# Performance work log

Hardware: AMD Instinct MI355X
Metric: run time of the kernel (lower is better)

The kernel has to match this reference:

```python
import jax, jax.numpy as jnp
import numpy as np

N_NODES = 50000
N_EDGES = 800000
IN_NODE = 128
IN_EDGE = 64
HEADS = 8
OUT_DIM = 8
HID = HEADS * OUT_DIM


def setup_inputs() -> dict:
    key = jax.random.key(0)
    ks = jax.random.split(key, 12)
    s = 1.0 / np.sqrt(IN_NODE)
    se = 1.0 / np.sqrt(IN_EDGE)
    return {
        "edge_index": jax.random.randint(ks[0], (2, N_EDGES), 0, N_NODES, dtype=jnp.int64),
        "h": jax.random.normal(ks[1], (N_NODES, IN_NODE), dtype=jnp.float32),
        "e": jax.random.normal(ks[2], (N_EDGES, IN_EDGE), dtype=jnp.float32),
        "WQ": jax.random.normal(ks[3], (IN_NODE, HID), dtype=jnp.float32) * s,
        "bQ": jnp.zeros((HID,), dtype=jnp.float32),
        "WK": jax.random.normal(ks[4], (IN_NODE, HID), dtype=jnp.float32) * s,
        "bK": jnp.zeros((HID,), dtype=jnp.float32),
        "WV": jax.random.normal(ks[5], (IN_NODE, HID), dtype=jnp.float32) * s,
        "bV": jnp.zeros((HID,), dtype=jnp.float32),
        "We": jax.random.normal(ks[6], (IN_EDGE, HID), dtype=jnp.float32) * se,
        "be": jnp.zeros((HID,), dtype=jnp.float32),
    }


def reference(edge_index, h, e, WQ, bQ, WK, bK, WV, bV, We, be):
    n = h.shape[0]
    # node projections -> [N, H, D]
    Q = (h @ WQ + bQ).reshape(-1, HEADS, OUT_DIM)
    K = (h @ WK + bK).reshape(-1, HEADS, OUT_DIM)
    V = (h @ WV + bV).reshape(-1, HEADS, OUT_DIM)
    pe = (e @ We + be).reshape(-1, HEADS, OUT_DIM)  # [E, H, D]

    src = edge_index[0]
    dst = edge_index[1]

    # per-edge attention score: K[src] * Q[dst] / sqrt(D) + proj_e
    score = (K[src] * Q[dst]) / np.sqrt(OUT_DIM) + pe  # [E, H, D]
    e_out = score
    a = jnp.exp(jnp.clip(score.sum(-1, keepdims=True), -5.0, 5.0))  # [E, H, 1]

    # scatter-sum of weighted V and scatter-mean of attention weights (by src)
    wV = jax.ops.segment_sum(V[src] * a, src, num_segments=n)       # [N, H, D]
    z_sum = jax.ops.segment_sum(a, src, num_segments=n)             # [N, H, 1]
    cnt = jax.ops.segment_sum(jnp.ones((src.shape[0],), a.dtype), src, num_segments=n)
    z = z_sum / jnp.maximum(cnt, 1.0)[:, None, None]                # scatter-mean

    h_out = wV / (z + 1e-06)
    return (h_out, e_out)
```

## Files before the change

### kernel.cpp

```cpp
#include <hip/hip_runtime.h>
#include <hip/hip_bf16.h>

typedef float  f32x4  __attribute__((ext_vector_type(4)));
typedef short  bf16x8 __attribute__((ext_vector_type(8)));

#define HEADS 8
#define HID 64
#define IN_NODE 128
#define IN_EDGE 64
#define LDSP 68

static __device__ __forceinline__ short f2bf(float f) {
    unsigned u = __builtin_bit_cast(unsigned, f);
    unsigned r = (u + 0x7FFFu + ((u >> 16) & 1u)) >> 16;
    return (short)r;
}

__global__ __launch_bounds__(256, 4) void qkv_kernel(
    const float* __restrict__ h,
    const float* __restrict__ WQ, const float* __restrict__ bQ,
    const float* __restrict__ WK, const float* __restrict__ bK,
    const float* __restrict__ WV, const float* __restrict__ bV,
    float* __restrict__ Q, float* __restrict__ K, float* __restrict__ V,
    int n_nodes)
{
    const int lane = threadIdx.x & 63;
    const int r16  = lane & 15;
    const int g4   = lane >> 4;
    const int wave   = blockIdx.x * (blockDim.x >> 6) + (threadIdx.x >> 6);
    const int nwaves = gridDim.x * (blockDim.x >> 6);
    const int mat  = blockIdx.y;

    const float* __restrict__ W  = (mat == 0) ? WQ : (mat == 1) ? WK : WV;
    const float* __restrict__ bp = (mat == 0) ? bQ : (mat == 1) ? bK : bV;
    float* __restrict__ out      = (mat == 0) ? Q  : (mat == 1) ? K  : V;

    bf16x8 bfr[4][4];
#pragma unroll
    for (int ct = 0; ct < 4; ++ct)
#pragma unroll
        for (int kc = 0; kc < 4; ++kc)
#pragma unroll
            for (int j = 0; j < 8; ++j) {
                int k = kc * 32 + g4 * 8 + j;
                bfr[ct][kc][j] = f2bf(W[k * HID + ct * 16 + r16]);
            }
    float bias[4];
#pragma unroll
    for (int ct = 0; ct < 4; ++ct) bias[ct] = bp[ct * 16 + r16];

    const int ntiles = (n_nodes + 15) >> 4;
    for (int tile = wave; tile < ntiles; tile += nwaves) {
        const int row0 = tile * 16;
        int arow = row0 + r16; if (arow > n_nodes - 1) arow = n_nodes - 1;
        const float* ap = h + (size_t)arow * IN_NODE + g4 * 8;

        bf16x8 afr[4];
#pragma unroll
        for (int kc = 0; kc < 4; ++kc) {
            f32x4 p0 = *reinterpret_cast<const f32x4*>(ap + kc * 32);
            f32x4 p1 = *reinterpret_cast<const f32x4*>(ap + kc * 32 + 4);
            afr[kc][0] = f2bf(p0.x); afr[kc][1] = f2bf(p0.y);
            afr[kc][2] = f2bf(p0.z); afr[kc][3] = f2bf(p0.w);
            afr[kc][4] = f2bf(p1.x); afr[kc][5] = f2bf(p1.y);
            afr[kc][6] = f2bf(p1.z); afr[kc][7] = f2bf(p1.w);
        }

        f32x4 acc[4] = {};
#pragma unroll
        for (int ct = 0; ct < 4; ++ct)
#pragma unroll
            for (int kc = 0; kc < 4; ++kc)
                acc[ct] = __builtin_amdgcn_mfma_f32_16x16x32_bf16(
                    afr[kc], bfr[ct][kc], acc[ct], 0, 0, 0);

#pragma unroll
        for (int ct = 0; ct < 4; ++ct)
#pragma unroll
            for (int r = 0; r < 4; ++r) {
                int orow = row0 + g4 * 4 + r;
                if (orow < n_nodes)
                    out[(size_t)orow * HID + ct * 16 + r16] = acc[ct][r] + bias[ct];
            }
    }
}

__global__ __launch_bounds__(256, 4) void edge_kernel(
    const int* __restrict__ ei, const float* __restrict__ e,
    const float* __restrict__ We, const float* __restrict__ be,
    const float* __restrict__ Q, const float* __restrict__ K,
    float* __restrict__ e_out, float* __restrict__ z_sum,
    float* __restrict__ cnt, int n_edges)
{
    const int lane = threadIdx.x & 63;
    const int wid  = threadIdx.x >> 6;
    const int r16  = lane & 15;
    const int g4   = lane >> 4;
    const int el   = lane >> 2;
    const int qg   = lane & 3;

    __shared__ float plds[4][16][LDSP];
    float (*my)[LDSP] = plds[wid];

    const int wave   = blockIdx.x * 4 + wid;
    const int nwaves = gridDim.x * 4;

    bf16x8 bfr[4][2];
#pragma unroll
    for (int ct = 0; ct < 4; ++ct)
#pragma unroll
        for (int kc = 0; kc < 2; ++kc)
#pragma unroll
            for (int j = 0; j < 8; ++j) {
                int k = kc * 32 + g4 * 8 + j;
                bfr[ct][kc][j] = f2bf(We[k * HID + ct * 16 + r16]);
            }
    float bias[4];
#pragma unroll
    for (int ct = 0; ct < 4; ++ct) bias[ct] = be[ct * 16 + r16];

    const float SC = 0.35355339059327373f;
    const int ntiles = (n_edges + 15) >> 4;
    for (int tile = wave; tile < ntiles; tile += nwaves) {
        const int e0 = tile * 16;

        int arow = e0 + r16; if (arow > n_edges - 1) arow = n_edges - 1;
        const float* ap = e + (size_t)arow * IN_EDGE + g4 * 8;
        f32x4 p0a = __builtin_nontemporal_load(reinterpret_cast<const f32x4*>(ap));
        f32x4 p1a = __builtin_nontemporal_load(reinterpret_cast<const f32x4*>(ap + 4));
        f32x4 p0b = __builtin_nontemporal_load(reinterpret_cast<const f32x4*>(ap + 32));
        f32x4 p1b = __builtin_nontemporal_load(reinterpret_cast<const f32x4*>(ap + 36));

        bf16x8 afr[2];
        afr[0][0] = f2bf(p0a.x); afr[0][1] = f2bf(p0a.y);
        afr[0][2] = f2bf(p0a.z); afr[0][3] = f2bf(p0a.w);
        afr[0][4] = f2bf(p1a.x); afr[0][5] = f2bf(p1a.y);
        afr[0][6] = f2bf(p1a.z); afr[0][7] = f2bf(p1a.w);
        afr[1][0] = f2bf(p0b.x); afr[1][1] = f2bf(p0b.y);
        afr[1][2] = f2bf(p0b.z); afr[1][3] = f2bf(p0b.w);
        afr[1][4] = f2bf(p1b.x); afr[1][5] = f2bf(p1b.y);
        afr[1][6] = f2bf(p1b.z); afr[1][7] = f2bf(p1b.w);

        f32x4 acc[4] = {};
#pragma unroll
        for (int ct = 0; ct < 4; ++ct) {
            acc[ct] = __builtin_amdgcn_mfma_f32_16x16x32_bf16(afr[0], bfr[ct][0], acc[ct], 0, 0, 0);
            acc[ct] = __builtin_amdgcn_mfma_f32_16x16x32_bf16(afr[1], bfr[ct][1], acc[ct], 0, 0, 0);
        }

#pragma unroll
        for (int ct = 0; ct < 4; ++ct)
#pragma unroll
            for (int r = 0; r < 4; ++r)
                my[g4 * 4 + r][ct * 16 + r16] = acc[ct][r] + bias[ct];

        int erow = e0 + el;
        bool valid = erow < n_edges;
        int erc = valid ? erow : n_edges - 1;
        int src = ei[erc];
        int dst = ei[n_edges + erc];

        const float* Kp = K + (size_t)src * HID + qg * 16;
        const float* Qp = Q + (size_t)dst * HID + qg * 16;
        f32x4 k0 = *reinterpret_cast<const f32x4*>(Kp);
        f32x4 k1 = *reinterpret_cast<const f32x4*>(Kp + 4);
        f32x4 k2 = *reinterpret_cast<const f32x4*>(Kp + 8);
        f32x4 k3 = *reinterpret_cast<const f32x4*>(Kp + 12);
        f32x4 q0 = *reinterpret_cast<const f32x4*>(Qp);
        f32x4 q1 = *reinterpret_cast<const f32x4*>(Qp + 4);
        f32x4 q2 = *reinterpret_cast<const f32x4*>(Qp + 8);
        f32x4 q3 = *reinterpret_cast<const f32x4*>(Qp + 12);

        asm volatile("s_waitcnt lgkmcnt(0)" ::: "memory");
        const float* mrow = &my[el][qg * 16];
        f32x4 p0 = *reinterpret_cast<const f32x4*>(mrow);
        f32x4 p1 = *reinterpret_cast<const f32x4*>(mrow + 4);
        f32x4 p2 = *reinterpret_cast<const f32x4*>(mrow + 8);
        f32x4 p3 = *reinterpret_cast<const f32x4*>(mrow + 12);

        f32x4 s0 = k0 * q0 * SC + p0;
        f32x4 s1 = k1 * q1 * SC + p1;
        f32x4 s2 = k2 * q2 * SC + p2;
        f32x4 s3 = k3 * q3 * SC + p3;

        if (valid) {
            float* op = e_out + (size_t)erow * HID + qg * 16;
            __builtin_nontemporal_store(s0, reinterpret_cast<f32x4*>(op));
            __builtin_nontemporal_store(s1, reinterpret_cast<f32x4*>(op + 4));
            __builtin_nontemporal_store(s2, reinterpret_cast<f32x4*>(op + 8));
            __builtin_nontemporal_store(s3, reinterpret_cast<f32x4*>(op + 12));
        }

        float hs0 = ((s0.x + s0.y) + (s0.z + s0.w)) + ((s1.x + s1.y) + (s1.z + s1.w));
        float hs1 = ((s2.x + s2.y) + (s2.z + s2.w)) + ((s3.x + s3.y) + (s3.z + s3.w));
        float a0 = __expf(fminf(fmaxf(hs0, -5.0f), 5.0f));
        float a1 = __expf(fminf(fmaxf(hs1, -5.0f), 5.0f));
        if (valid) {
            atomicAdd(&z_sum[src * HEADS + qg * 2], a0);
            atomicAdd(&z_sum[src * HEADS + qg * 2 + 1], a1);
            if (qg == 0) atomicAdd(&cnt[src], 1.0f);
        }
    }
}

__global__ __launch_bounds__(256) void finalize_kernel(
    const float* __restrict__ V, const float* __restrict__ z_sum,
    const float* __restrict__ cnt, float* __restrict__ h_out, int total)
{
    int i = blockIdx.x * 256 + threadIdx.x;
    if (i >= total) return;
    int node = i >> 6;
    int head = (i >> 3) & 7;
    float S = z_sum[node * HEADS + head];
    float c = fmaxf(cnt[node], 1.0f);
    h_out[i] = V[i] * S / (S / c + 1e-6f);
}

extern "C" void kernel_launch(void* const* d_in, const int* in_sizes, int n_in,
                              void* d_out, int out_size, void* d_ws, size_t ws_size,
                              hipStream_t stream)
{
    const int*   ei = (const int*)d_in[0];
    const float* h  = (const float*)d_in[1];
    const float* e  = (const float*)d_in[2];
    const float* WQ = (const float*)d_in[3];
    const float* bQ = (const float*)d_in[4];
    const float* WK = (const float*)d_in[5];
    const float* bK = (const float*)d_in[6];
    const float* WV = (const float*)d_in[7];
    const float* bV = (const float*)d_in[8];
    const float* We = (const float*)d_in[9];
    const float* be = (const float*)d_in[10];

    const int n_nodes = in_sizes[1] / IN_NODE;
    const int n_edges = in_sizes[2] / IN_EDGE;

    float* out_h = (float*)d_out;
    float* out_e = out_h + (size_t)n_nodes * HID;

    float* Q     = (float*)d_ws;
    float* K     = Q + (size_t)n_nodes * HID;
    float* V     = K + (size_t)n_nodes * HID;
    float* z_sum = V + (size_t)n_nodes * HID;
    float* cnt   = z_sum + (size_t)n_nodes * HEADS;

    (void)hipMemsetAsync(z_sum, 0, (size_t)n_nodes * (HEADS + 1) * sizeof(float), stream);

    {
        dim3 grid(96, 3);
        qkv_kernel<<<grid, 256, 0, stream>>>(h, WQ, bQ, WK, bK, WV, bV,
                                             Q, K, V, n_nodes);
    }
    {
        edge_kernel<<<2048, 256, 0, stream>>>(ei, e, We, be, Q, K,
                                              out_e, z_sum, cnt, n_edges);
    }
    {
        const int total = n_nodes * HID;
        finalize_kernel<<<(total + 255) / 256, 256, 0, stream>>>(V, z_sum, cnt,
                                                                 out_h, total);
    }
}
```

Before: 243.7 us.

## Split scatter atomics out of edge kernel into separate z-pass kernel

```diff
diff --git a/kernel.cpp b/kernel.cpp
--- a/kernel.cpp
+++ b/kernel.cpp
@@ -1,6 +1,7 @@
 #include <hip/hip_runtime.h>
 #include <hip/hip_bf16.h>
 
+typedef float  f32x2  __attribute__((ext_vector_type(2)));
 typedef float  f32x4  __attribute__((ext_vector_type(4)));
 typedef short  bf16x8 __attribute__((ext_vector_type(8)));
 
@@ -89,8 +90,7 @@
     const int* __restrict__ ei, const float* __restrict__ e,
     const float* __restrict__ We, const float* __restrict__ be,
     const float* __restrict__ Q, const float* __restrict__ K,
-    float* __restrict__ e_out, float* __restrict__ z_sum,
-    float* __restrict__ cnt, int n_edges)
+    float* __restrict__ e_out, float* __restrict__ aws, int n_edges)
 {
     const int lane = threadIdx.x & 63;
     const int wid  = threadIdx.x >> 6;
@@ -183,23 +183,57 @@
         f32x4 s2 = k2 * q2 * SC + p2;
         f32x4 s3 = k3 * q3 * SC + p3;
 
+        float hs0 = ((s0.x + s0.y) + (s0.z + s0.w)) + ((s1.x + s1.y) + (s1.z + s1.w));
+        float hs1 = ((s2.x + s2.y) + (s2.z + s2.w)) + ((s3.x + s3.y) + (s3.z + s3.w));
+        float a0 = __expf(fminf(fmaxf(hs0, -5.0f), 5.0f));
+        float a1 = __expf(fminf(fmaxf(hs1, -5.0f), 5.0f));
+
         if (valid) {
             float* op = e_out + (size_t)erow * HID + qg * 16;
             __builtin_nontemporal_store(s0, reinterpret_cast<f32x4*>(op));
             __builtin_nontemporal_store(s1, reinterpret_cast<f32x4*>(op + 4));
             __builtin_nontemporal_store(s2, reinterpret_cast<f32x4*>(op + 8));
             __builtin_nontemporal_store(s3, reinterpret_cast<f32x4*>(op + 12));
+            f32x2 av = {a0, a1};
+            *reinterpret_cast<f32x2*>(aws + (size_t)erow * HEADS + qg * 2) = av;
         }
-
-        float hs0 = ((s0.x + s0.y) + (s0.z + s0.w)) + ((s1.x + s1.y) + (s1.z + s1.w));
-        float hs1 = ((s2.x + s2.y) + (s2.z + s2.w)) + ((s3.x + s3.y) + (s3.z + s3.w));
-        float a0 = __expf(fminf(fmaxf(hs0, -5.0f), 5.0f));
-        float a1 = __expf(fminf(fmaxf(hs1, -5.0f), 5.0f));
-        if (valid) {
-            atomicAdd(&z_sum[src * HEADS + qg * 2], a0);
-            atomicAdd(&z_sum[src * HEADS + qg * 2 + 1], a1);
-            if (qg == 0) atomicAdd(&cnt[src], 1.0f);
+    }
+}
+
+__global__ __launch_bounds__(256) void zpass_kernel(
+    const int* __restrict__ ei, const float* __restrict__ aws,
+    float* __restrict__ z_sum, float* __restrict__ cnt, int n_edges)
+{
+    const int tid  = blockIdx.x * 256 + threadIdx.x;
+    const int nthr = gridDim.x * 256;
+    const int head = tid & 7;
+    const int eg   = tid >> 3;
+    const int estr = nthr >> 3;
+
+    int edge = eg;
+    for (; edge + 3 * estr < n_edges; edge += 4 * estr) {
+        int e0 = edge, e1 = edge + estr, e2 = edge + 2 * estr, e3 = edge + 3 * estr;
+        int s0 = ei[e0], s1 = ei[e1], s2 = ei[e2], s3 = ei[e3];
+        float v0 = aws[(size_t)e0 * HEADS + head];
+        float v1 = aws[(size_t)e1 * HEADS + head];
+        float v2 = aws[(size_t)e2 * HEADS + head];
+        float v3 = aws[(size_t)e3 * HEADS + head];
+        atomicAdd(&z_sum[s0 * HEADS + head], v0);
+        atomicAdd(&z_sum[s1 * HEADS + head], v1);
+        atomicAdd(&z_sum[s2 * HEADS + head], v2);
+        atomicAdd(&z_sum[s3 * HEADS + head], v3);
+        if (head == 0) {
+            atomicAdd(&cnt[s0], 1.0f);
+            atomicAdd(&cnt[s1], 1.0f);
+            atomicAdd(&cnt[s2], 1.0f);
+            atomicAdd(&cnt[s3], 1.0f);
         }
+    }
+    for (; edge < n_edges; edge += estr) {
+        int s = ei[edge];
+        float v = aws[(size_t)edge * HEADS + head];
+        atomicAdd(&z_sum[s * HEADS + head], v);
+        if (head == 0) atomicAdd(&cnt[s], 1.0f);
     }
 }
 
@@ -243,6 +277,7 @@
     float* V     = K + (size_t)n_nodes * HID;
     float* z_sum = V + (size_t)n_nodes * HID;
     float* cnt   = z_sum + (size_t)n_nodes * HEADS;
+    float* aws   = cnt + (size_t)n_nodes;
 
     (void)hipMemsetAsync(z_sum, 0, (size_t)n_nodes * (HEADS + 1) * sizeof(float), stream);
 
@@ -253,7 +288,10 @@
     }
     {
         edge_kernel<<<2048, 256, 0, stream>>>(ei, e, We, be, Q, K,
-                                              out_e, z_sum, cnt, n_edges);
+                                              out_e, aws, n_edges);
+    }
+    {
+        zpass_kernel<<<2048, 256, 0, stream>>>(ei, aws, z_sum, cnt, n_edges);
     }
     {
         const int total = n_nodes * HID;
```

Measured after the change: 333.5 us. 1.37x slower.
